# Optimization experiments

Measured on AMD Instinct MI355X. Metric: run time of the kernel, lower is better.

Reference implementation:

```python
import jax, jax.numpy as jnp
import numpy as np

DIM = 16
HID = 32

def setup_inputs() -> dict:
    key = jax.random.key(0)
    ks = jax.random.split(key, 5)
    B, S = 32768, 64
    x = jax.random.normal(ks[0], (B, S, DIM), dtype=jnp.float32)
    # LayerNorm params (torch defaults: weight=1, bias=0)
    ln_w = jnp.ones((DIM,), dtype=jnp.float32)
    ln_b = jnp.zeros((DIM,), dtype=jnp.float32)
    # Linear params, torch-style init scale ~ 1/sqrt(fan_in)
    w1 = jax.random.uniform(ks[1], (HID, DIM), jnp.float32, -1.0, 1.0) / np.sqrt(DIM)
    b1 = jax.random.uniform(ks[2], (HID,), jnp.float32, -1.0, 1.0) / np.sqrt(DIM)
    w2 = jax.random.uniform(ks[3], (DIM, HID), jnp.float32, -1.0, 1.0) / np.sqrt(HID)
    b2 = jax.random.uniform(ks[4], (DIM,), jnp.float32, -1.0, 1.0) / np.sqrt(HID)
    return {"x": x, "ln_w": ln_w, "ln_b": ln_b, "w1": w1, "b1": b1, "w2": w2, "b2": b2}

def _layernorm(x, w, b, eps=1e-5):
    mu = jnp.mean(x, axis=-1, keepdims=True)
    var = jnp.mean(jnp.square(x - mu), axis=-1, keepdims=True)
    return (x - mu) * jax.lax.rsqrt(var + eps) * w + b

def reference(x, ln_w, ln_b, w1, b1, w2, b2):
    h = _layernorm(x, ln_w, ln_b)
    h = jnp.einsum('bsd,hd->bsh', h, w1) + b1
    h = jax.nn.gelu(h, approximate=False)  # torch nn.GELU default is exact erf
    h = jnp.einsum('bsh,dh->bsd', h, w2) + b2
    return x + h
```

## Files before the change

### kernel.cpp

```cpp
#include <hip/hip_runtime.h>
#include <math.h>

#define DIM 16
#define HID 32

typedef float  f32x4  __attribute__((ext_vector_type(4)));
typedef float  v2f    __attribute__((ext_vector_type(2)));
typedef short  bf16x8 __attribute__((ext_vector_type(8)));

__device__ inline unsigned short f2bf(float f) {
    union { float f; unsigned u; } v; v.f = f;
    unsigned r = v.u + 0x7fffu + ((v.u >> 16) & 1u);
    return (unsigned short)(r >> 16);
}

__device__ inline unsigned cvt_pk_bf16(float lo, float hi) {
    unsigned r;
    asm("v_cvt_pk_bf16_f32 %0, %1, %2" : "=v"(r) : "v"(lo), "v"(hi));
    return r;
}

__device__ inline v2f gelu2(v2f h) {
    v2f hh  = h * (v2f){0.5f, 0.5f};
    v2f ahh = __builtin_elementwise_abs(hh);
    v2f az  = ahh * (v2f){1.41421356237309505f, 1.41421356237309505f};
    v2f den = __builtin_elementwise_fma(az, (v2f){0.3275911f, 0.3275911f},
                                        (v2f){1.0f, 1.0f});
    v2f t   = (v2f){__builtin_amdgcn_rcpf(den.x), __builtin_amdgcn_rcpf(den.y)};
    v2f h2  = h * h;
    v2f ex  = h2 * (v2f){-0.721347520444482f, -0.721347520444482f};
    v2f e   = (v2f){__builtin_amdgcn_exp2f(ex.x), __builtin_amdgcn_exp2f(ex.y)};
    v2f p   = __builtin_elementwise_fma(t, (v2f){1.061405429f, 1.061405429f},
                                        (v2f){-1.453152027f, -1.453152027f});
    p = __builtin_elementwise_fma(t, p, (v2f){1.421413741f, 1.421413741f});
    p = __builtin_elementwise_fma(t, p, (v2f){-0.284496736f, -0.284496736f});
    p = __builtin_elementwise_fma(t, p, (v2f){0.254829592f, 0.254829592f});
    p = p * t;
    v2f erfa = __builtin_elementwise_fma(-p, e, (v2f){1.0f, 1.0f});
    return __builtin_elementwise_fma(ahh, erfa, hh);
}

__global__ __launch_bounds__(256) void fused_ln_mlp_mfma(
    const float* __restrict__ x,
    const float* __restrict__ ln_w,
    const float* __restrict__ ln_b,
    const float* __restrict__ w1,
    const float* __restrict__ b1,
    const float* __restrict__ w2,
    const float* __restrict__ b2,
    float* __restrict__ out,
    int nrows)
{
    const int tid  = threadIdx.x;
    const int lane = tid & 63;
    const int wave = tid >> 6;
    const int q    = lane >> 4;
    const int c    = lane & 15;
    const int rowbase = (blockIdx.x * 4 + wave) * 64;
    (void)nrows;

    bf16x8 aW1[2];
    #pragma unroll
    for (int t = 0; t < 2; t++) {
        bf16x8 f = {0, 0, 0, 0, 0, 0, 0, 0};
        const float* wp = w1 + (16 * t + c) * DIM + 4 * q;
        #pragma unroll
        for (int j = 0; j < 4; j++)
            ((unsigned short*)&f)[j] = f2bf(wp[j]);
        aW1[t] = f;
    }
    bf16x8 aW2;
    {
        const float* wp = w2 + c * HID;
        #pragma unroll
        for (int j = 0; j < 8; j++) {
            int hid = (j < 4) ? (4 * q + j) : (16 + 4 * q + (j - 4));
            ((unsigned short*)&aW2)[j] = f2bf(wp[hid]);
        }
    }
    const f32x4 b1q0 = *(const f32x4*)(b1 + 4 * q);
    const f32x4 b1q1 = *(const f32x4*)(b1 + 16 + 4 * q);
    const f32x4 b2q  = *(const f32x4*)(b2 + 4 * q);
    const f32x4 lnw4 = *(const f32x4*)(ln_w + 4 * q);
    const f32x4 lnb4 = *(const f32x4*)(ln_b + 4 * q);

    f32x4 xv[4];
    #pragma unroll
    for (int rc = 0; rc < 4; rc++)
        xv[rc] = *(const f32x4*)(x + (size_t)(rowbase + rc * 16 + c) * DIM + 4 * q);

    #pragma unroll
    for (int rc = 0; rc < 4; rc++) {
        const f32x4 v = xv[rc];

        float s  = (v.x + v.y) + (v.z + v.w);
        float ss = fmaf(v.x, v.x, fmaf(v.y, v.y, fmaf(v.z, v.z, v.w * v.w)));
        s  += __shfl_xor(s, 16);  ss += __shfl_xor(ss, 16);
        s  += __shfl_xor(s, 32);  ss += __shfl_xor(ss, 32);
        float mu  = s * (1.0f / DIM);
        float var = fmaf(-mu, mu, ss * (1.0f / DIM));
        float a   = __builtin_amdgcn_rsqf(var + 1e-5f);

        f32x4 aw  = lnw4 * a;
        f32x4 muv = {mu, mu, mu, mu};
        f32x4 off = __builtin_elementwise_fma(-muv, aw, lnb4);
        f32x4 xn  = __builtin_elementwise_fma(v, aw, off);

        union { unsigned u[4]; bf16x8 f; } bX;
        bX.u[0] = cvt_pk_bf16(xn.x, xn.y);
        bX.u[1] = cvt_pk_bf16(xn.z, xn.w);
        bX.u[2] = 0u;
        bX.u[3] = 0u;

        const f32x4 z = {0.f, 0.f, 0.f, 0.f};
        f32x4 h0 = __builtin_amdgcn_mfma_f32_16x16x32_bf16(aW1[0], bX.f, z, 0, 0, 0) + b1q0;
        f32x4 h1 = __builtin_amdgcn_mfma_f32_16x16x32_bf16(aW1[1], bX.f, z, 0, 0, 0) + b1q1;

        v2f g0 = gelu2((v2f){h0.x, h0.y});
        v2f g1 = gelu2((v2f){h0.z, h0.w});
        v2f g2 = gelu2((v2f){h1.x, h1.y});
        v2f g3 = gelu2((v2f){h1.z, h1.w});
        union { unsigned u[4]; bf16x8 f; } bP;
        bP.u[0] = cvt_pk_bf16(g0.x, g0.y);
        bP.u[1] = cvt_pk_bf16(g1.x, g1.y);
        bP.u[2] = cvt_pk_bf16(g2.x, g2.y);
        bP.u[3] = cvt_pk_bf16(g3.x, g3.y);

        f32x4 acc = __builtin_amdgcn_mfma_f32_16x16x32_bf16(aW2, bP.f, z, 0, 0, 0);

        f32x4 o = acc + b2q + v;
        size_t base = (size_t)(rowbase + rc * 16 + c) * DIM + 4 * q;
        __builtin_nontemporal_store(o, (f32x4*)(out + base));
    }
}

extern "C" void kernel_launch(void* const* d_in, const int* in_sizes, int n_in,
                              void* d_out, int out_size, void* d_ws, size_t ws_size,
                              hipStream_t stream) {
    const float* x    = (const float*)d_in[0];
    const float* ln_w = (const float*)d_in[1];
    const float* ln_b = (const float*)d_in[2];
    const float* w1   = (const float*)d_in[3];
    const float* b1   = (const float*)d_in[4];
    const float* w2   = (const float*)d_in[5];
    const float* b2   = (const float*)d_in[6];
    float* out = (float*)d_out;

    int nrows = in_sizes[0] / DIM;
    int rows_per_block = 256;
    int grid = (nrows + rows_per_block - 1) / rows_per_block;

    fused_ln_mlp_mfma<<<grid, 256, 0, stream>>>(
        x, ln_w, ln_b, w1, b1, w2, b2, out, nrows);
}
```

Baseline: 234.7 us.

## Process 256 rows per wave with deeper load batching and software bf16 packing

Each wave now handles 256 rows instead of 64, issuing 16 vector loads up front and amortizing weight conversion and setup over more rows. The grid shrinks fourfold, launch bounds gain a min-blocks hint, and an early exit guards against waves past the row count. The inline-asm packed bf16 conversion is replaced with a software round-to-nearest-even pack, which costs more ALU work per element. The larger register array for x raises register pressure, which may reduce occupancy.

After: 250.5 us. 6.7% more time.

```diff
diff --git a/kernel.cpp b/kernel.cpp
--- a/kernel.cpp
+++ b/kernel.cpp
@@ -13,11 +13,8 @@
     unsigned r = v.u + 0x7fffu + ((v.u >> 16) & 1u);
     return (unsigned short)(r >> 16);
 }
-
-__device__ inline unsigned cvt_pk_bf16(float lo, float hi) {
-    unsigned r;
-    asm("v_cvt_pk_bf16_f32 %0, %1, %2" : "=v"(r) : "v"(lo), "v"(hi));
-    return r;
+__device__ inline unsigned packbf(float lo, float hi) {
+    return (unsigned)f2bf(lo) | ((unsigned)f2bf(hi) << 16);
 }
 
 __device__ inline v2f gelu2(v2f h) {
@@ -40,7 +37,7 @@
     return __builtin_elementwise_fma(ahh, erfa, hh);
 }
 
-__global__ __launch_bounds__(256) void fused_ln_mlp_mfma(
+__global__ __launch_bounds__(256, 4) void fused_ln_mlp_mfma(
     const float* __restrict__ x,
     const float* __restrict__ ln_w,
     const float* __restrict__ ln_b,
@@ -56,8 +53,9 @@
     const int wave = tid >> 6;
     const int q    = lane >> 4;
     const int c    = lane & 15;
-    const int rowbase = (blockIdx.x * 4 + wave) * 64;
-    (void)nrows;
+
+    const int wavebase = (blockIdx.x * 4 + wave) * 256;
+    if (wavebase >= nrows) return;
 
     bf16x8 aW1[2];
     #pragma unroll
@@ -84,14 +82,14 @@
     const f32x4 lnw4 = *(const f32x4*)(ln_w + 4 * q);
     const f32x4 lnb4 = *(const f32x4*)(ln_b + 4 * q);
 
-    f32x4 xv[4];
+    f32x4 xv[16];
     #pragma unroll
-    for (int rc = 0; rc < 4; rc++)
-        xv[rc] = *(const f32x4*)(x + (size_t)(rowbase + rc * 16 + c) * DIM + 4 * q);
+    for (int t = 0; t < 16; t++)
+        xv[t] = *(const f32x4*)(x + (size_t)(wavebase + t * 16 + c) * DIM + 4 * q);
 
     #pragma unroll
-    for (int rc = 0; rc < 4; rc++) {
-        const f32x4 v = xv[rc];
+    for (int t = 0; t < 16; t++) {
+        const f32x4 v = xv[t];
 
         float s  = (v.x + v.y) + (v.z + v.w);
         float ss = fmaf(v.x, v.x, fmaf(v.y, v.y, fmaf(v.z, v.z, v.w * v.w)));
@@ -107,8 +105,8 @@
         f32x4 xn  = __builtin_elementwise_fma(v, aw, off);
 
         union { unsigned u[4]; bf16x8 f; } bX;
-        bX.u[0] = cvt_pk_bf16(xn.x, xn.y);
-        bX.u[1] = cvt_pk_bf16(xn.z, xn.w);
+        bX.u[0] = packbf(xn.x, xn.y);
+        bX.u[1] = packbf(xn.z, xn.w);
         bX.u[2] = 0u;
         bX.u[3] = 0u;
 
@@ -121,15 +119,15 @@
         v2f g2 = gelu2((v2f){h1.x, h1.y});
         v2f g3 = gelu2((v2f){h1.z, h1.w});
         union { unsigned u[4]; bf16x8 f; } bP;
-        bP.u[0] = cvt_pk_bf16(g0.x, g0.y);
-        bP.u[1] = cvt_pk_bf16(g1.x, g1.y);
-        bP.u[2] = cvt_pk_bf16(g2.x, g2.y);
-        bP.u[3] = cvt_pk_bf16(g3.x, g3.y);
+        bP.u[0] = packbf(g0.x, g0.y);
+        bP.u[1] = packbf(g1.x, g1.y);
+        bP.u[2] = packbf(g2.x, g2.y);
+        bP.u[3] = packbf(g3.x, g3.y);
 
         f32x4 acc = __builtin_amdgcn_mfma_f32_16x16x32_bf16(aW2, bP.f, z, 0, 0, 0);
 
         f32x4 o = acc + b2q + v;
-        size_t base = (size_t)(rowbase + rc * 16 + c) * DIM + 4 * q;
+        size_t base = (size_t)(wavebase + t * 16 + c) * DIM + 4 * q;
         __builtin_nontemporal_store(o, (f32x4*)(out + base));
     }
 }
@@ -147,7 +145,7 @@
     float* out = (float*)d_out;
 
     int nrows = in_sizes[0] / DIM;
-    int rows_per_block = 256;
+    int rows_per_block = 1024;
     int grid = (nrows + rows_per_block - 1) / rows_per_block;
 
     fused_ln_mlp_mfma<<<grid, 256, 0, stream>>>(
```
